# Kernel optimization log

Measured on AMD Instinct MI355X. Metric: run time of the kernel, lower is better.

The kernel has to match this reference:

```python
import jax, jax.numpy as jnp
import numpy as np

BATCH, SEQ, HID, OUT = 4, 4096, 4096, 4096
N_ADAPTERS, RANK = 8, 64
ALPHA = 1.0


def setup_inputs() -> dict:
    key = jax.random.key(0)
    k1, k2, k3, k4 = jax.random.split(key, 4)
    x = jax.random.normal(k1, (BATCH, SEQ, HID), dtype=jnp.float32)
    adapter_ids = jax.random.randint(k2, (BATCH,), 0, N_ADAPTERS, dtype=jnp.int32)
    # A: per-adapter up-projection (n_adapters, rank, out); original init randn*0.02
    A = jax.random.normal(k3, (N_ADAPTERS, RANK, OUT), dtype=jnp.float32) * 0.02
    # B: per-adapter down-projection (hid, n_adapters, rank); original init is zeros,
    # use small random values so the baseline output is non-trivial.
    B = jax.random.normal(k4, (HID, N_ADAPTERS, RANK), dtype=jnp.float32) * 0.02
    return {"x": x, "adapter_ids": adapter_ids, "A": A, "B": B}


def reference(x, adapter_ids, A, B):
    # Equivalent dense math of the stk block-sparse sdd+dsd:
    # out[b] = (x[b] @ B[:, a, :]) @ A[a] * (alpha / rank),  a = adapter_ids[b]
    n_adapters, rank, out_f = A.shape
    B_sel = jnp.take(B, adapter_ids, axis=1)       # (hid, batch, rank)
    A_sel = jnp.take(A, adapter_ids, axis=0)       # (batch, rank, out)
    Bx = jnp.einsum('bsh,hbr->bsr', x, B_sel)      # sampled-dense-dense
    out = jnp.einsum('bsr,bro->bso', Bx, A_sel)    # dense-sparse-dense
    scaling = jnp.asarray(ALPHA / rank, dtype=out.dtype)
    return out * scaling
```

## Files before the change

### kernel.cpp

```cpp
#include <hip/hip_runtime.h>

#define BATCH 4
#define SEQ   4096
#define HID   4096
#define OUTF  4096
#define NA    8
#define RANK  64

typedef __attribute__((ext_vector_type(8))) short  short8;
typedef __attribute__((ext_vector_type(4))) float  f32x4;

__device__ __forceinline__ unsigned short cvt_bf16(float f) {
  return (unsigned short)((__float_as_uint(f) + 0x8000u) >> 16);
}
__device__ __forceinline__ unsigned int pack_bf16_2(float lo, float hi) {
  unsigned int a = __float_as_uint(lo);
  unsigned int b = __float_as_uint(hi);
  return ((a + 0x8000u) >> 16) | ((b + 0x8000u) & 0xFFFF0000u);
}

__global__ __launch_bounds__(256) void prep_kernel(
    const float* __restrict__ A, const float* __restrict__ Bm,
    unsigned short* __restrict__ Bct, unsigned short* __restrict__ Act) {
  __shared__ unsigned short lds[64 * 72];
  int bid = blockIdx.x;
  int t   = threadIdx.x;
  int lo  = t & 63;
  int hi4 = t >> 6;
  if (bid < 512) {
    int a  = bid >> 6;
    int h0 = (bid & 63) << 6;
    #pragma unroll
    for (int p = 0; p < 16; ++p) {
      int hl = (p << 2) + hi4;
      float v = Bm[((size_t)(h0 + hl) * NA + a) * RANK + lo];
      lds[lo * 72 + hl] = cvt_bf16(v);
    }
    __syncthreads();
    #pragma unroll
    for (int p = 0; p < 16; ++p) {
      int rl = (p << 2) + hi4;
      Bct[((size_t)a * RANK + rl) * HID + h0 + lo] = lds[rl * 72 + lo];
    }
  } else {
    int b2 = bid - 512;
    int a  = b2 >> 6;
    int o0 = (b2 & 63) << 6;
    #pragma unroll
    for (int p = 0; p < 16; ++p) {
      int rl = (p << 2) + hi4;
      float v = A[((size_t)a * RANK + rl) * OUTF + o0 + lo];
      lds[lo * 72 + rl] = cvt_bf16(v);
    }
    __syncthreads();
    #pragma unroll
    for (int p = 0; p < 16; ++p) {
      int ol = (p << 2) + hi4;
      Act[((size_t)a * OUTF + o0 + ol) * RANK + lo] = lds[ol * 72 + lo];
    }
  }
}

__global__ __launch_bounds__(512, 8) void fused_kernel(
    const float* __restrict__ x, const int* __restrict__ ids,
    const unsigned short* __restrict__ Bct, const unsigned short* __restrict__ Act,
    float* __restrict__ out) {
  __shared__ float red[8 * 16 * 65];
  __shared__ unsigned short bx[16 * 72];
  int bid   = blockIdx.x;
  int batch = bid & 3;
  int s0    = (bid >> 2) << 4;
  int t     = threadIdx.x;
  int w     = t >> 6;
  int lane  = t & 63;
  int m     = lane & 15;
  int q     = lane >> 4;
  int a     = ids[batch];

  const float* xrow = x + (size_t)(batch * SEQ + s0 + m) * HID;
  const unsigned short* bbase = Bct + (size_t)a * RANK * HID;

  f32x4 acc[4];
  #pragma unroll
  for (int nt = 0; nt < 4; ++nt) acc[nt] = (f32x4){0.f, 0.f, 0.f, 0.f};

  int kw = w << 9;
  for (int it = 0; it < 16; ++it) {
    int k = kw + (it << 5) + (q << 3);
    f32x4 f0 = __builtin_nontemporal_load((const f32x4*)(xrow + k));
    f32x4 f1 = __builtin_nontemporal_load((const f32x4*)(xrow + k + 4));
    union { short8 v; unsigned int u[4]; } af;
    af.u[0] = pack_bf16_2(f0[0], f0[1]);
    af.u[1] = pack_bf16_2(f0[2], f0[3]);
    af.u[2] = pack_bf16_2(f1[0], f1[1]);
    af.u[3] = pack_bf16_2(f1[2], f1[3]);
    #pragma unroll
    for (int nt = 0; nt < 4; ++nt) {
      short8 bf = *(const short8*)(bbase + (size_t)(nt * 16 + m) * HID + k);
      acc[nt] = __builtin_amdgcn_mfma_f32_16x16x32_bf16(af.v, bf, acc[nt], 0, 0, 0);
    }
  }

  #pragma unroll
  for (int nt = 0; nt < 4; ++nt)
    #pragma unroll
    for (int r = 0; r < 4; ++r)
      red[(w * 16 + q * 4 + r) * 65 + nt * 16 + m] = acc[nt][r];
  __syncthreads();

  if (t < 256) {
    int row = t >> 4;
    int rb  = (t & 15) << 2;
    float v0 = 0.f, v1 = 0.f, v2 = 0.f, v3 = 0.f;
    #pragma unroll
    for (int ww = 0; ww < 8; ++ww) {
      const float* rr = &red[(ww * 16 + row) * 65 + rb];
      v0 += rr[0]; v1 += rr[1]; v2 += rr[2]; v3 += rr[3];
    }
    const float sc = 1.0f / 64.0f;
    uint2 pk;
    pk.x = pack_bf16_2(v0 * sc, v1 * sc);
    pk.y = pack_bf16_2(v2 * sc, v3 * sc);
    *(uint2*)&bx[row * 72 + rb] = pk;
  }
  __syncthreads();

  short8 p0 = *(const short8*)&bx[m * 72 + (q << 3)];
  short8 p1 = *(const short8*)&bx[m * 72 + 32 + (q << 3)];
  const unsigned short* abase = Act + (size_t)a * OUTF * RANK;
  float* orow = out + (size_t)(batch * SEQ + s0 + m) * OUTF;

  for (int i = 0; i < 8; ++i) {
    int o0 = ((w << 3) + i) << 6;
    #pragma unroll
    for (int nt = 0; nt < 4; ++nt) {
      const unsigned short* arow = abase + (size_t)(o0 + nt * 16 + m) * RANK;
      short8 b0 = *(const short8*)(arow + (q << 3));
      short8 b1 = *(const short8*)(arow + 32 + (q << 3));
      f32x4 c = (f32x4){0.f, 0.f, 0.f, 0.f};
      c = __builtin_amdgcn_mfma_f32_16x16x32_bf16(b0, p0, c, 0, 0, 0);
      c = __builtin_amdgcn_mfma_f32_16x16x32_bf16(b1, p1, c, 0, 0, 0);
      *(f32x4*)(orow + o0 + nt * 16 + (q << 2)) = c;
    }
  }
}

extern "C" void kernel_launch(void* const* d_in, const int* in_sizes, int n_in,
                              void* d_out, int out_size, void* d_ws, size_t ws_size,
                              hipStream_t stream) {
  const float* x   = (const float*)d_in[0];
  const int*   ids = (const int*)d_in[1];
  const float* A   = (const float*)d_in[2];
  const float* Bm  = (const float*)d_in[3];
  float*       out = (float*)d_out;

  unsigned short* Bct = (unsigned short*)d_ws;
  unsigned short* Act = Bct + (size_t)NA * RANK * HID;

  prep_kernel <<<1024, 256, 0, stream>>>(A, Bm, Bct, Act);
  fused_kernel<<<1024, 512, 0, stream>>>(x, ids, Bct, Act, out);
}
```

Measured before the change: 556.6 us.

## Stage x loads and output stores through swizzled LDS for coalesced global access

The x tile is now loaded cooperatively with fully contiguous per-row 16-byte accesses, converted to bf16 and stored into an XOR-swizzled LDS buffer, then read back as MFMA fragments. Output tiles are likewise written to swizzled LDS first and then streamed to global memory in contiguous row segments. The goal is to replace the strided per-lane global loads and scattered 16-byte stores with coalesced transactions. In exchange it adds extra barriers per chunk and LDS round trips, and serialises load and compute phases within a block.

```diff
diff --git a/kernel.cpp b/kernel.cpp
--- a/kernel.cpp
+++ b/kernel.cpp
@@ -9,6 +9,7 @@
 
 typedef __attribute__((ext_vector_type(8))) short  short8;
 typedef __attribute__((ext_vector_type(4))) float  f32x4;
+typedef __attribute__((ext_vector_type(2))) unsigned int u32x2;
 
 __device__ __forceinline__ unsigned short cvt_bf16(float f) {
   return (unsigned short)((__float_as_uint(f) + 0x8000u) >> 16);
@@ -65,8 +66,12 @@
     const float* __restrict__ x, const int* __restrict__ ids,
     const unsigned short* __restrict__ Bct, const unsigned short* __restrict__ Act,
     float* __restrict__ out) {
-  __shared__ float red[8 * 16 * 65];
+  __shared__ float smem[8 * 16 * 65];
   __shared__ unsigned short bx[16 * 72];
+  unsigned short* xs = (unsigned short*)smem;
+  float*          os = smem;
+  float*          red = smem;
+
   int bid   = blockIdx.x;
   int batch = bid & 3;
   int s0    = (bid >> 2) << 4;
@@ -77,29 +82,50 @@
   int q     = lane >> 4;
   int a     = ids[batch];
 
-  const float* xrow = x + (size_t)(batch * SEQ + s0 + m) * HID;
+  const float* xg = x + (size_t)(batch * SEQ + s0) * HID;
   const unsigned short* bbase = Bct + (size_t)a * RANK * HID;
 
   f32x4 acc[4];
   #pragma unroll
   for (int nt = 0; nt < 4; ++nt) acc[nt] = (f32x4){0.f, 0.f, 0.f, 0.f};
 
-  int kw = w << 9;
-  for (int it = 0; it < 16; ++it) {
-    int k = kw + (it << 5) + (q << 3);
-    f32x4 f0 = __builtin_nontemporal_load((const f32x4*)(xrow + k));
-    f32x4 f1 = __builtin_nontemporal_load((const f32x4*)(xrow + k + 4));
-    union { short8 v; unsigned int u[4]; } af;
-    af.u[0] = pack_bf16_2(f0[0], f0[1]);
-    af.u[1] = pack_bf16_2(f0[2], f0[3]);
-    af.u[2] = pack_bf16_2(f1[0], f1[1]);
-    af.u[3] = pack_bf16_2(f1[2], f1[3]);
-    #pragma unroll
-    for (int nt = 0; nt < 4; ++nt) {
-      short8 bf = *(const short8*)(bbase + (size_t)(nt * 16 + m) * HID + k);
-      acc[nt] = __builtin_amdgcn_mfma_f32_16x16x32_bf16(af.v, bf, acc[nt], 0, 0, 0);
-    }
-  }
+  for (int kc = 0; kc < 4; ++kc) {
+    if (kc) __syncthreads();
+    f32x4 v[8];
+    #pragma unroll
+    for (int r = 0; r < 8; ++r) {
+      int flat = (r << 11) + (t << 2);
+      int row  = flat >> 10;
+      int col  = flat & 1023;
+      v[r] = __builtin_nontemporal_load(
+          (const f32x4*)(xg + (size_t)row * HID + (kc << 10) + col));
+    }
+    #pragma unroll
+    for (int r = 0; r < 8; ++r) {
+      int flat = (r << 11) + (t << 2);
+      int row  = flat >> 10;
+      int col  = flat & 1023;
+      int csw  = (col >> 3) ^ (row & 7);
+      u32x2 pk;
+      pk[0] = pack_bf16_2(v[r][0], v[r][1]);
+      pk[1] = pack_bf16_2(v[r][2], v[r][3]);
+      *(u32x2*)&xs[row * 1024 + (csw << 3) + (col & 7)] = pk;
+    }
+    __syncthreads();
+    #pragma unroll
+    for (int j = 0; j < 4; ++j) {
+      int kl  = (w << 7) + (j << 5) + (q << 3);
+      int csw = (kl >> 3) ^ (m & 7);
+      short8 af = *(const short8*)&xs[m * 1024 + (csw << 3)];
+      int kglob = (kc << 10) + kl;
+      #pragma unroll
+      for (int nt = 0; nt < 4; ++nt) {
+        short8 bf = *(const short8*)(bbase + (size_t)(nt * 16 + m) * HID + kglob);
+        acc[nt] = __builtin_amdgcn_mfma_f32_16x16x32_bf16(af, bf, acc[nt], 0, 0, 0);
+      }
+    }
+  }
+  __syncthreads();
 
   #pragma unroll
   for (int nt = 0; nt < 4; ++nt)
@@ -128,20 +154,32 @@
   short8 p0 = *(const short8*)&bx[m * 72 + (q << 3)];
   short8 p1 = *(const short8*)&bx[m * 72 + 32 + (q << 3)];
   const unsigned short* abase = Act + (size_t)a * OUTF * RANK;
-  float* orow = out + (size_t)(batch * SEQ + s0 + m) * OUTF;
-
-  for (int i = 0; i < 8; ++i) {
-    int o0 = ((w << 3) + i) << 6;
+
+  for (int oc = 0; oc < 8; ++oc) {
+    int o0 = oc << 9;
     #pragma unroll
     for (int nt = 0; nt < 4; ++nt) {
-      const unsigned short* arow = abase + (size_t)(o0 + nt * 16 + m) * RANK;
+      const unsigned short* arow =
+          abase + (size_t)(o0 + (w << 6) + nt * 16 + m) * RANK;
       short8 b0 = *(const short8*)(arow + (q << 3));
       short8 b1 = *(const short8*)(arow + 32 + (q << 3));
-      f32x4 c = (f32x4){0.f, 0.f, 0.f, 0.f};
-      c = __builtin_amdgcn_mfma_f32_16x16x32_bf16(b0, p0, c, 0, 0, 0);
-      c = __builtin_amdgcn_mfma_f32_16x16x32_bf16(b1, p1, c, 0, 0, 0);
-      *(f32x4*)(orow + o0 + nt * 16 + (q << 2)) = c;
-    }
+      f32x4 cc = (f32x4){0.f, 0.f, 0.f, 0.f};
+      cc = __builtin_amdgcn_mfma_f32_16x16x32_bf16(b0, p0, cc, 0, 0, 0);
+      cc = __builtin_amdgcn_mfma_f32_16x16x32_bf16(b1, p1, cc, 0, 0, 0);
+      int ci  = (w << 4) + (nt << 2) + q;
+      *(f32x4*)&os[m * 512 + ((ci ^ (m & 7)) << 2)] = cc;
+    }
+    __syncthreads();
+    #pragma unroll
+    for (int r = 0; r < 4; ++r) {
+      int flat = (r << 11) + (t << 2);
+      int row  = flat >> 9;
+      int col  = flat & 511;
+      int csw  = (col >> 2) ^ (row & 7);
+      f32x4 vv = *(const f32x4*)&os[row * 512 + (csw << 2)];
+      *(f32x4*)(out + (size_t)(batch * SEQ + s0 + row) * OUTF + o0 + col) = vv;
+    }
+    __syncthreads();
   }
 }
 
```

After: 565.9 us. No clear change (+1.7%).
